# Optimization experiments

Measured on AMD Instinct MI355X. Metric: run time of the kernel, lower is better.

The kernel has to match this reference:

```python
import jax, jax.numpy as jnp
import numpy as np

N = 50000   # nodes
E = 300000  # edges
D = 256     # emb_dim
L = 5       # num_layers
BN_EPS = 1e-5


def setup_inputs() -> dict:
    key = jax.random.key(0)
    ks = jax.random.split(key, 6)
    scale = 0.05
    return {
        "x": jax.random.normal(ks[0], (N, D), jnp.float32),
        "src": jax.random.randint(ks[1], (E,), 0, N, dtype=jnp.int32),
        "dst": jax.random.randint(ks[2], (E,), 0, N, dtype=jnp.int32),
        "W1": jax.random.normal(ks[3], (L, D, D), jnp.float32) * scale,
        "b1": jnp.zeros((L, D), jnp.float32),
        "g1": jnp.ones((L, D), jnp.float32),
        "bt1": jnp.zeros((L, D), jnp.float32),
        "W2": jax.random.normal(ks[4], (L, D, D), jnp.float32) * scale,
        "b2": jnp.zeros((L, D), jnp.float32),
        "eps": jnp.zeros((L,), jnp.float32),
        "bn_g": jnp.ones((L, D), jnp.float32),
        "bn_b": jnp.zeros((L, D), jnp.float32),
    }


def _bn(h, gamma, beta):
    # torch BatchNorm1d training-mode forward: biased batch stats over nodes
    mean = jnp.mean(h, axis=0)
    var = jnp.var(h, axis=0)
    return (h - mean) * jax.lax.rsqrt(var + BN_EPS) * gamma + beta


def reference(x, src, dst, W1, b1, g1, bt1, W2, b2, eps, bn_g, bn_b):
    h = x
    for l in range(L):
        # GINConv: gather relu(x[src]) -> scatter-sum to dst
        msg = jax.nn.relu(h[src])                          # [E, D]
        agg = jax.ops.segment_sum(msg, dst, num_segments=N)  # [N, D]
        z = (1.0 + eps[l]) * h + agg
        # mlp: Linear -> BN -> ReLU -> Linear
        z = z @ W1[l] + b1[l]
        z = jax.nn.relu(_bn(z, g1[l], bt1[l]))
        z = z @ W2[l] + b2[l]
        # per-layer BatchNorm; dropout is identity (eval / drop_ratio=0)
        z = _bn(z, bn_g[l], bn_b[l])
        if l < L - 1:
            z = jax.nn.relu(z)
        h = z
    return h  # JK='last'
```

## Files before the change

### kernel.cpp

```cpp
#include <hip/hip_runtime.h>
#include <hip/hip_bf16.h>

#define N_NODES 50000
#define N_EDGES 300000
#define DIM 256
#define MPAD 50048

typedef __attribute__((ext_vector_type(8))) _Float16 half8;
typedef __attribute__((ext_vector_type(4))) _Float16 half4;
typedef __attribute__((ext_vector_type(4))) float f32x4;

__device__ __forceinline__ void async16(const void* g, void* l) {
    __builtin_amdgcn_global_load_lds(
        (const __attribute__((address_space(1))) unsigned int*)g,
        (__attribute__((address_space(3))) unsigned int*)l, 16, 0, 0);
}

__global__ __launch_bounds__(256) void hist_dst(const int* __restrict__ dst,
                                                int* __restrict__ deg, int E) {
    int e = blockIdx.x * blockDim.x + threadIdx.x;
    if (e < E) atomicAdd(&deg[dst[e]], 1);
}

__global__ __launch_bounds__(1024) void scan_blk(const int* __restrict__ deg,
                                                 int* __restrict__ ptr,
                                                 int* __restrict__ bsum, int n) {
    __shared__ int wsum[16];
    __shared__ int wpre[16];
    int tid = threadIdx.x;
    int i = blockIdx.x * 1024 + tid;
    int v = (i < n) ? deg[i] : 0;
    int lane = tid & 63, w = tid >> 6;
    int s = v;
#pragma unroll
    for (int off = 1; off < 64; off <<= 1) {
        int t = __shfl_up(s, off, 64);
        if (lane >= off) s += t;
    }
    if (lane == 63) wsum[w] = s;
    __syncthreads();
    if (tid < 16) {
        int acc = 0;
        for (int j = 0; j < tid; j++) acc += wsum[j];
        wpre[tid] = acc;
    }
    __syncthreads();
    int incl = s + wpre[w];
    if (i < n) ptr[i] = incl - v;
    if (tid == 1023) bsum[blockIdx.x] = incl;
}

__global__ __launch_bounds__(64) void scan_top(int* __restrict__ bsum,
                                               int* __restrict__ ptr,
                                               int nb, int n, int E) {
    int lane = threadIdx.x;
    int v = (lane < nb) ? bsum[lane] : 0;
    int s = v;
#pragma unroll
    for (int off = 1; off < 64; off <<= 1) {
        int t = __shfl_up(s, off, 64);
        if (lane >= off) s += t;
    }
    if (lane < nb) bsum[lane] = s - v;
    if (lane == 0) ptr[n] = E;
}

__global__ __launch_bounds__(1024) void scan_add(int* __restrict__ ptr,
                                                 const int* __restrict__ bsum,
                                                 int* __restrict__ cursor, int n) {
    int i = blockIdx.x * 1024 + threadIdx.x;
    if (i < n) {
        int val = ptr[i] + bsum[blockIdx.x];
        ptr[i] = val;
        cursor[i] = val;
    }
}

__global__ __launch_bounds__(256) void scatter_src(const int* __restrict__ src,
                                                   const int* __restrict__ dst,
                                                   int* __restrict__ cursor,
                                                   int* __restrict__ srcbuf, int E) {
    int e = blockIdx.x * blockDim.x + threadIdx.x;
    if (e < E) {
        int pos = atomicAdd(&cursor[dst[e]], 1);
        srcbuf[pos] = src[e];
    }
}

__global__ __launch_bounds__(256) void x2h(const float* __restrict__ x,
                                           _Float16* __restrict__ hb) {
    size_t i = (size_t)blockIdx.x * 256 + threadIdx.x;
    float4 v = ((const float4*)x)[i];
    half4 o;
    o.x = (_Float16)v.x; o.y = (_Float16)v.y;
    o.z = (_Float16)v.z; o.w = (_Float16)v.w;
    ((half4*)hb)[i] = o;
}

__global__ __launch_bounds__(256) void wconv(const float* __restrict__ W1,
                                             const float* __restrict__ W2,
                                             _Float16* __restrict__ Wt) {
    int mat = blockIdx.x >> 4;
    int t = blockIdx.x & 15;
    int tr = t >> 2, tc = t & 3;
    const float* W = (mat < 5) ? (W1 + (size_t)mat * 65536)
                               : (W2 + (size_t)(mat - 5) * 65536);
    __shared__ float tile[64][65];
    int tid = threadIdx.x;
    int c = tid & 63, r0 = tid >> 6;
#pragma unroll 4
    for (int i = 0; i < 16; i++) {
        int r = r0 + i * 4;
        tile[r][c] = W[(size_t)(tr * 64 + r) * 256 + tc * 64 + c];
    }
    __syncthreads();
    _Float16* o = Wt + (size_t)mat * 65536;
#pragma unroll 4
    for (int i = 0; i < 16; i++) {
        int r = r0 + i * 4;
        o[(size_t)(tc * 64 + r) * 256 + tr * 64 + c] = (_Float16)tile[c][r];
    }
}

__global__ __launch_bounds__(256) void gather_h(const _Float16* __restrict__ h,
                                                const int* __restrict__ ptr,
                                                const int* __restrict__ srcbuf,
                                                _Float16* __restrict__ z,
                                                const float* __restrict__ eps) {
    int node = blockIdx.x * 4 + (threadIdx.x >> 6);
    if (node >= N_NODES) return;
    int lane = threadIdx.x & 63;
    int beg = ptr[node], end = ptr[node + 1];
    float s = 1.0f + eps[0];
    half4 hv = ((const half4*)(h + (size_t)node * DIM))[lane];
    float a0 = (float)hv.x * s, a1 = (float)hv.y * s;
    float a2 = (float)hv.z * s, a3 = (float)hv.w * s;
    int e = beg;
    for (; e + 4 <= end; e += 4) {
        int s0 = srcbuf[e], s1 = srcbuf[e + 1], s2 = srcbuf[e + 2], s3 = srcbuf[e + 3];
        half4 v0 = ((const half4*)(h + (size_t)s0 * DIM))[lane];
        half4 v1 = ((const half4*)(h + (size_t)s1 * DIM))[lane];
        half4 v2 = ((const half4*)(h + (size_t)s2 * DIM))[lane];
        half4 v3 = ((const half4*)(h + (size_t)s3 * DIM))[lane];
        a0 += fmaxf((float)v0.x, 0.f) + fmaxf((float)v1.x, 0.f)
            + fmaxf((float)v2.x, 0.f) + fmaxf((float)v3.x, 0.f);
        a1 += fmaxf((float)v0.y, 0.f) + fmaxf((float)v1.y, 0.f)
            + fmaxf((float)v2.y, 0.f) + fmaxf((float)v3.y, 0.f);
        a2 += fmaxf((float)v0.z, 0.f) + fmaxf((float)v1.z, 0.f)
            + fmaxf((float)v2.z, 0.f) + fmaxf((float)v3.z, 0.f);
        a3 += fmaxf((float)v0.w, 0.f) + fmaxf((float)v1.w, 0.f)
            + fmaxf((float)v2.w, 0.f) + fmaxf((float)v3.w, 0.f);
    }
    for (; e < end; e++) {
        half4 v = ((const half4*)(h + (size_t)srcbuf[e] * DIM))[lane];
        a0 += fmaxf((float)v.x, 0.f); a1 += fmaxf((float)v.y, 0.f);
        a2 += fmaxf((float)v.z, 0.f); a3 += fmaxf((float)v.w, 0.f);
    }
    half4 o;
    o.x = (_Float16)a0; o.y = (_Float16)a1;
    o.z = (_Float16)a2; o.w = (_Float16)a3;
    ((half4*)(z + (size_t)node * DIM))[lane] = o;
}

__global__ __launch_bounds__(256) void gather_bn(const _Float16* __restrict__ C,
                                                 const int* __restrict__ ptr,
                                                 const int* __restrict__ srcbuf,
                                                 _Float16* __restrict__ z,
                                                 const float* __restrict__ scsh,
                                                 const float* __restrict__ eps,
                                                 int l) {
    int node = blockIdx.x * 4 + (threadIdx.x >> 6);
    if (node >= N_NODES) return;
    int lane = threadIdx.x & 63;
    float4 sc = ((const float4*)scsh)[lane];
    float4 sh = ((const float4*)(scsh + DIM))[lane];
    int beg = ptr[node], end = ptr[node + 1];
    float s = 1.0f + eps[l];
    half4 hv = ((const half4*)(C + (size_t)node * DIM))[lane];
    float a0 = s * fmaxf((float)hv.x * sc.x + sh.x, 0.f);
    float a1 = s * fmaxf((float)hv.y * sc.y + sh.y, 0.f);
    float a2 = s * fmaxf((float)hv.z * sc.z + sh.z, 0.f);
    float a3 = s * fmaxf((float)hv.w * sc.w + sh.w, 0.f);
    int e = beg;
    for (; e + 4 <= end; e += 4) {
        int s0 = srcbuf[e], s1 = srcbuf[e + 1], s2 = srcbuf[e + 2], s3 = srcbuf[e + 3];
        half4 v0 = ((const half4*)(C + (size_t)s0 * DIM))[lane];
        half4 v1 = ((const half4*)(C + (size_t)s1 * DIM))[lane];
        half4 v2 = ((const half4*)(C + (size_t)s2 * DIM))[lane];
        half4 v3 = ((const half4*)(C + (size_t)s3 * DIM))[lane];
        a0 += fmaxf((float)v0.x * sc.x + sh.x, 0.f) + fmaxf((float)v1.x * sc.x + sh.x, 0.f)
            + fmaxf((float)v2.x * sc.x + sh.x, 0.f) + fmaxf((float)v3.x * sc.x + sh.x, 0.f);
        a1 += fmaxf((float)v0.y * sc.y + sh.y, 0.f) + fmaxf((float)v1.y * sc.y + sh.y, 0.f)
            + fmaxf((float)v2.y * sc.y + sh.y, 0.f) + fmaxf((float)v3.y * sc.y + sh.y, 0.f);
        a2 += fmaxf((float)v0.z * sc.z + sh.z, 0.f) + fmaxf((float)v1.z * sc.z + sh.z, 0.f)
            + fmaxf((float)v2.z * sc.z + sh.z, 0.f) + fmaxf((float)v3.z * sc.z + sh.z, 0.f);
        a3 += fmaxf((float)v0.w * sc.w + sh.w, 0.f) + fmaxf((float)v1.w * sc.w + sh.w, 0.f)
            + fmaxf((float)v2.w * sc.w + sh.w, 0.f) + fmaxf((float)v3.w * sc.w + sh.w, 0.f);
    }
    for (; e < end; e++) {
        half4 v = ((const half4*)(C + (size_t)srcbuf[e] * DIM))[lane];
        a0 += fmaxf((float)v.x * sc.x + sh.x, 0.f);
        a1 += fmaxf((float)v.y * sc.y + sh.y, 0.f);
        a2 += fmaxf((float)v.z * sc.z + sh.z, 0.f);
        a3 += fmaxf((float)v.w * sc.w + sh.w, 0.f);
    }
    half4 o;
    o.x = (_Float16)a0; o.y = (_Float16)a1;
    o.z = (_Float16)a2; o.w = (_Float16)a3;
    ((half4*)(z + (size_t)node * DIM))[lane] = o;
}

#define GEMM_EPILOGUE                                                        \
    __syncthreads();                                                         \
    float* colsum = (float*)((char*)smem + 49152);                           \
    float* colsq = colsum + 128;                                             \
    if (tid < 128) { colsum[tid] = 0.0f; colsq[tid] = 0.0f; }                \
    _Float16* Cs = (_Float16*)smem;                                          \
    float bcol[4];                                                           \
    _Pragma("unroll")                                                        \
    for (int j = 0; j < 4; j++) bcol[j] = bias[col0 + wn + j * 16 + lrow];   \
    float csum[4] = {0.f, 0.f, 0.f, 0.f};                                    \
    float csq[4] = {0.f, 0.f, 0.f, 0.f};                                     \
    _Pragma("unroll")                                                        \
    for (int i = 0; i < 4; i++) {                                            \
        int rl = wm + i * 16 + quad * 4;                                     \
        _Pragma("unroll")                                                    \
        for (int j = 0; j < 4; j++) {                                        \
            int cl = wn + j * 16 + lrow;                                     \
            _Pragma("unroll")                                                \
            for (int r = 0; r < 4; r++) {                                    \
                float v = acc[i][j][r] + bcol[j];                            \
                Cs[(rl + r) * 136 + cl] = (_Float16)v;                       \
                if (row0 + rl + r < M) { csum[j] += v; csq[j] += v * v; }    \
            }                                                                \
        }                                                                    \
    }                                                                        \
    __syncthreads();                                                         \
    {                                                                        \
        int rgrp = lane >> 4, ch = lane & 15;                                \
        _Pragma("unroll")                                                    \
        for (int it = 0; it < 8; it++) {                                     \
            int row = wid * 32 + it * 4 + rgrp;                              \
            uint4 vv = *(const uint4*)(Cs + row * 136 + ch * 8);             \
            *(uint4*)(C + (size_t)(row0 + row) * DIM + col0 + ch * 8) = vv;  \
        }                                                                    \
    }                                                                        \
    _Pragma("unroll")                                                        \
    for (int j = 0; j < 4; j++) {                                            \
        atomicAdd(&colsum[wn + j * 16 + lrow], csum[j]);                     \
        atomicAdd(&colsq[wn + j * 16 + lrow], csq[j]);                       \
    }                                                                        \
    __syncthreads();                                                         \
    if (tid < 128) {                                                         \
        float* st = stats + (blockIdx.y & 7) * 512;                          \
        atomicAdd(&st[col0 + tid], colsum[tid]);                             \
        atomicAdd(&st[DIM + col0 + tid], colsq[tid]);                        \
    }

__global__ __launch_bounds__(256) void gemm_f16(const _Float16* __restrict__ A,
                                                const _Float16* __restrict__ Wt,
                                                const float* __restrict__ bias,
                                                _Float16* __restrict__ C,
                                                float* __restrict__ stats,
                                                int M) {
    __shared__ uint4 smem[4096];

    int tid = threadIdx.x;
    int wid = tid >> 6, lane = tid & 63;
    int quad = lane >> 4, lrow = lane & 15;
    int row0 = blockIdx.y * 128, col0 = blockIdx.x * 128;
    int wm = (wid & 1) * 64, wn = (wid >> 1) * 64;

    f32x4 acc[4][4] = {};
    const char* Ab = (const char*)A;
    const char* Bb = (const char*)Wt;

#pragma unroll
    for (int ko = 0; ko < 2; ko++) {
        int kb0 = ko * 256;
#pragma unroll
        for (int j = 0; j < 8; j++) {
            int sbase = wid * 512 + j * 64;
            int s = sbase + lane;
            int m = s >> 4;
            int c = (s & 15) ^ (m & 7);
            size_t go = (size_t)(row0 + m) * 512 + kb0 + c * 16;
            async16(Ab + go, (char*)smem + sbase * 16);
            size_t gob = (size_t)(col0 + m) * 512 + kb0 + c * 16;
            async16(Bb + gob, (char*)smem + 32768 + sbase * 16);
        }
        __syncthreads();
#pragma unroll
        for (int kc = 0; kc < 4; kc++) {
            half8 af[4], bf[4];
#pragma unroll
            for (int t = 0; t < 4; t++) {
                int ma = wm + t * 16 + lrow;
                int ca = kc * 4 + quad;
                af[t] = *(const half8*)((const char*)smem +
                                        (ma * 16 + (ca ^ (ma & 7))) * 16);
                int mb = wn + t * 16 + lrow;
                bf[t] = *(const half8*)((const char*)smem + 32768 +
                                        (mb * 16 + (ca ^ (mb & 7))) * 16);
            }
#pragma unroll
            for (int i = 0; i < 4; i++)
#pragma unroll
                for (int j2 = 0; j2 < 4; j2++)
                    acc[i][j2] = __builtin_amdgcn_mfma_f32_16x16x32_f16(
                        af[i], bf[j2], acc[i][j2], 0, 0, 0);
        }
        if (ko == 0) __syncthreads();
    }

    GEMM_EPILOGUE
}

__global__ __launch_bounds__(256) void gemm_bn(const _Float16* __restrict__ A,
                                               const _Float16* __restrict__ Wt,
                                               const float* __restrict__ bias,
                                               const float* __restrict__ scsh,
                                               _Float16* __restrict__ C,
                                               float* __restrict__ stats,
                                               int M) {
    __shared__ uint4 smem[4096];

    int tid = threadIdx.x;
    int wid = tid >> 6, lane = tid & 63;
    int quad = lane >> 4, lrow = lane & 15;
    int row0 = blockIdx.y * 128, col0 = blockIdx.x * 128;
    int wm = (wid & 1) * 64, wn = (wid >> 1) * 64;

    half8 scv[8], shv[8];
#pragma unroll
    for (int cc = 0; cc < 8; cc++) {
        int kk = cc * 32 + quad * 8;
        float4 s0 = *(const float4*)(scsh + kk);
        float4 s1 = *(const float4*)(scsh + kk + 4);
        float4 h0 = *(const float4*)(scsh + DIM + kk);
        float4 h1 = *(const float4*)(scsh + DIM + kk + 4);
        half8 sv = {(_Float16)s0.x, (_Float16)s0.y, (_Float16)s0.z, (_Float16)s0.w,
                    (_Float16)s1.x, (_Float16)s1.y, (_Float16)s1.z, (_Float16)s1.w};
        half8 hv = {(_Float16)h0.x, (_Float16)h0.y, (_Float16)h0.z, (_Float16)h0.w,
                    (_Float16)h1.x, (_Float16)h1.y, (_Float16)h1.z, (_Float16)h1.w};
        scv[cc] = sv;
        shv[cc] = hv;
    }

    f32x4 acc[4][4] = {};
    const char* Ab = (const char*)A;
    const char* Bb = (const char*)Wt;
    const half8 zerov = {0, 0, 0, 0, 0, 0, 0, 0};

#pragma unroll
    for (int ko = 0; ko < 2; ko++) {
        int kb0 = ko * 256;
#pragma unroll
        for (int j = 0; j < 8; j++) {
            int sbase = wid * 512 + j * 64;
            int s = sbase + lane;
            int m = s >> 4;
            int c = (s & 15) ^ (m & 7);
            size_t go = (size_t)(row0 + m) * 512 + kb0 + c * 16;
            async16(Ab + go, (char*)smem + sbase * 16);
            size_t gob = (size_t)(col0 + m) * 512 + kb0 + c * 16;
            async16(Bb + gob, (char*)smem + 32768 + sbase * 16);
        }
        __syncthreads();
#pragma unroll
        for (int kc = 0; kc < 4; kc++) {
            half8 af[4], bf[4];
            half8 sv = scv[ko * 4 + kc];
            half8 hv = shv[ko * 4 + kc];
#pragma unroll
            for (int t = 0; t < 4; t++) {
                int ma = wm + t * 16 + lrow;
                int ca = kc * 4 + quad;
                half8 a = *(const half8*)((const char*)smem +
                                          (ma * 16 + (ca ^ (ma & 7))) * 16);
                af[t] = __builtin_elementwise_max(a * sv + hv, zerov);
                int mb = wn + t * 16 + lrow;
                bf[t] = *(const half8*)((const char*)smem + 32768 +
                                        (mb * 16 + (ca ^ (mb & 7))) * 16);
            }
#pragma unroll
            for (int i = 0; i < 4; i++)
#pragma unroll
                for (int j2 = 0; j2 < 4; j2++)
                    acc[i][j2] = __builtin_amdgcn_mfma_f32_16x16x32_f16(
                        af[i], bf[j2], acc[i][j2], 0, 0, 0);
        }
        if (ko == 0) __syncthreads();
    }

    GEMM_EPILOGUE
}

__global__ __launch_bounds__(256) void bn_finalize(float* __restrict__ stats,
                                                   const float* __restrict__ g,
                                                   const float* __restrict__ beta,
                                                   float* __restrict__ scsh,
                                                   int n) {
    int d = threadIdx.x;
    float s = 0.0f, sq = 0.0f;
#pragma unroll
    for (int r = 0; r < 8; r++) {
        s += stats[r * 512 + d];
        sq += stats[r * 512 + 256 + d];
        stats[r * 512 + d] = 0.0f;
        stats[r * 512 + 256 + d] = 0.0f;
    }
    float invn = 1.0f / (float)n;
    float mean = s * invn;
    float var = sq * invn - mean * mean;
    float inv = rsqrtf(var + 1e-5f);
    float scale = g[d] * inv;
    scsh[d] = scale;
    scsh[DIM + d] = beta[d] - mean * scale;
}

__global__ __launch_bounds__(256) void bn_apply_f(const _Float16* __restrict__ in,
                                                  float* __restrict__ outf,
                                                  const float* __restrict__ scsh) {
    size_t i = (size_t)blockIdx.x * 256 + threadIdx.x;
    int c4 = (int)(i & 63);
    float4 sc = ((const float4*)scsh)[c4];
    float4 sh = ((const float4*)(scsh + DIM))[c4];
    half4 v = ((const half4*)in)[i];
    float4 o;
    o.x = (float)v.x * sc.x + sh.x;
    o.y = (float)v.y * sc.y + sh.y;
    o.z = (float)v.z * sc.z + sh.z;
    o.w = (float)v.w * sc.w + sh.w;
    ((float4*)outf)[i] = o;
}

extern "C" void kernel_launch(void* const* d_in, const int* in_sizes, int n_in,
                              void* d_out, int out_size, void* d_ws, size_t ws_size,
                              hipStream_t stream) {
    (void)in_sizes; (void)n_in; (void)out_size; (void)ws_size;
    const float* x   = (const float*)d_in[0];
    const int*   src = (const int*)d_in[1];
    const int*   dst = (const int*)d_in[2];
    const float* W1  = (const float*)d_in[3];
    const float* b1  = (const float*)d_in[4];
    const float* g1  = (const float*)d_in[5];
    const float* bt1 = (const float*)d_in[6];
    const float* W2  = (const float*)d_in[7];
    const float* b2  = (const float*)d_in[8];
    const float* eps = (const float*)d_in[9];
    const float* bng = (const float*)d_in[10];
    const float* bnb = (const float*)d_in[11];
    float* out = (float*)d_out;

    const int N = N_NODES, E = N_EDGES, D = DIM;
    size_t NDp = (size_t)MPAD * D;

    _Float16* gin  = (_Float16*)d_ws;
    _Float16* C1   = gin + NDp;
    _Float16* C2   = C1 + NDp;
    _Float16* Wt   = C2 + NDp;
    float* statsA = (float*)(Wt + 10 * 65536);
    float* statsB = statsA + 4096;
    float* scshA = statsB + 4096;
    float* scshB = scshA + 512;
    int* deg     = (int*)(scshB + 512);
    int* ptr     = deg + N;
    int* bsum    = ptr + N + 1;
    int* srcbuf  = bsum + 64;

    const int ELEM4_BLOCKS = N * D / 4 / 256;
    const int NODE_BLOCKS  = (N + 3) / 4;
    const int E_BLOCKS     = (E + 255) / 256;
    const int SCAN_BLOCKS  = (N + 1023) / 1024;
    const dim3 GEMM_GRID(2, MPAD / 128);

    hipMemsetAsync(deg, 0, N * sizeof(int), stream);
    hipMemsetAsync(statsA, 0, 8192 * sizeof(float), stream);
    hist_dst<<<E_BLOCKS, 256, 0, stream>>>(dst, deg, E);
    scan_blk<<<SCAN_BLOCKS, 1024, 0, stream>>>(deg, ptr, bsum, N);
    scan_top<<<1, 64, 0, stream>>>(bsum, ptr, SCAN_BLOCKS, N, E);
    scan_add<<<SCAN_BLOCKS, 1024, 0, stream>>>(ptr, bsum, deg, N);
    scatter_src<<<E_BLOCKS, 256, 0, stream>>>(src, dst, deg, srcbuf, E);
    wconv<<<160, 256, 0, stream>>>(W1, W2, Wt);
    x2h<<<ELEM4_BLOCKS, 256, 0, stream>>>(x, C1);

    for (int l = 0; l < 5; l++) {
        if (l == 0)
            gather_h<<<NODE_BLOCKS, 256, 0, stream>>>(C1, ptr, srcbuf, gin, eps);
        else
            gather_bn<<<NODE_BLOCKS, 256, 0, stream>>>(C2, ptr, srcbuf, gin,
                                                       scshB, eps, l);

        gemm_f16<<<GEMM_GRID, 256, 0, stream>>>(
            gin, Wt + (size_t)l * 65536, b1 + (size_t)l * D, C1, statsA, N);
        bn_finalize<<<1, 256, 0, stream>>>(statsA, g1 + (size_t)l * D,
                                           bt1 + (size_t)l * D, scshA, N);

        gemm_bn<<<GEMM_GRID, 256, 0, stream>>>(
            C1, Wt + (size_t)(5 + l) * 65536, b2 + (size_t)l * D, scshA,
            C2, statsB, N);
        bn_finalize<<<1, 256, 0, stream>>>(statsB, bng + (size_t)l * D,
                                           bnb + (size_t)l * D, scshB, N);

        if (l == 4)
            bn_apply_f<<<ELEM4_BLOCKS, 256, 0, stream>>>(C2, out, scshB);
    }
}
```

Baseline: 674.5 us.

## Shrink GEMM LDS tiles to K=64 chunks, merge setup kernels and memsets

The two GEMM kernels now stream K in four 64-element chunks instead of two 128-element chunks. This roughly halves their shared memory (about 35 KB instead of 64 KB) so more blocks can be resident per CU, at the cost of extra barriers and less work per load phase. Separately, the scan_top kernel is folded into scan_add, which now computes each block's prefix offset by a wave reduction. The weight-convert and x-to-fp16 kernels are merged into one launch, and the two memsets are combined by placing deg right after the stats buffers. Together these changes cut kernel launch count in the setup phase.

```diff
diff --git a/kernel.cpp b/kernel.cpp
--- a/kernel.cpp
+++ b/kernel.cpp
@@ -50,30 +50,26 @@
     if (tid == 1023) bsum[blockIdx.x] = incl;
 }
 
-__global__ __launch_bounds__(64) void scan_top(int* __restrict__ bsum,
-                                               int* __restrict__ ptr,
-                                               int nb, int n, int E) {
-    int lane = threadIdx.x;
-    int v = (lane < nb) ? bsum[lane] : 0;
-    int s = v;
-#pragma unroll
-    for (int off = 1; off < 64; off <<= 1) {
-        int t = __shfl_up(s, off, 64);
-        if (lane >= off) s += t;
-    }
-    if (lane < nb) bsum[lane] = s - v;
-    if (lane == 0) ptr[n] = E;
-}
-
 __global__ __launch_bounds__(1024) void scan_add(int* __restrict__ ptr,
                                                  const int* __restrict__ bsum,
-                                                 int* __restrict__ cursor, int n) {
-    int i = blockIdx.x * 1024 + threadIdx.x;
+                                                 int* __restrict__ cursor,
+                                                 int n, int E) {
+    __shared__ int soff;
+    int tid = threadIdx.x;
+    if (tid < 64) {
+        int v = (tid < (int)blockIdx.x) ? bsum[tid] : 0;
+#pragma unroll
+        for (int off = 32; off > 0; off >>= 1) v += __shfl_down(v, off, 64);
+        if (tid == 0) soff = v;
+    }
+    __syncthreads();
+    int i = blockIdx.x * 1024 + tid;
     if (i < n) {
-        int val = ptr[i] + bsum[blockIdx.x];
+        int val = ptr[i] + soff;
         ptr[i] = val;
         cursor[i] = val;
     }
+    if (i == n) ptr[n] = E;
 }
 
 __global__ __launch_bounds__(256) void scatter_src(const int* __restrict__ src,
@@ -87,38 +83,39 @@
     }
 }
 
-__global__ __launch_bounds__(256) void x2h(const float* __restrict__ x,
-                                           _Float16* __restrict__ hb) {
-    size_t i = (size_t)blockIdx.x * 256 + threadIdx.x;
-    float4 v = ((const float4*)x)[i];
-    half4 o;
-    o.x = (_Float16)v.x; o.y = (_Float16)v.y;
-    o.z = (_Float16)v.z; o.w = (_Float16)v.w;
-    ((half4*)hb)[i] = o;
-}
-
-__global__ __launch_bounds__(256) void wconv(const float* __restrict__ W1,
-                                             const float* __restrict__ W2,
-                                             _Float16* __restrict__ Wt) {
-    int mat = blockIdx.x >> 4;
-    int t = blockIdx.x & 15;
-    int tr = t >> 2, tc = t & 3;
-    const float* W = (mat < 5) ? (W1 + (size_t)mat * 65536)
-                               : (W2 + (size_t)(mat - 5) * 65536);
+__global__ __launch_bounds__(256) void prep(const float* __restrict__ W1,
+                                            const float* __restrict__ W2,
+                                            _Float16* __restrict__ Wt,
+                                            const float* __restrict__ x,
+                                            _Float16* __restrict__ hb) {
     __shared__ float tile[64][65];
     int tid = threadIdx.x;
-    int c = tid & 63, r0 = tid >> 6;
+    if (blockIdx.x < 160) {
+        int mat = blockIdx.x >> 4;
+        int t = blockIdx.x & 15;
+        int tr = t >> 2, tc = t & 3;
+        const float* W = (mat < 5) ? (W1 + (size_t)mat * 65536)
+                                   : (W2 + (size_t)(mat - 5) * 65536);
+        int c = tid & 63, r0 = tid >> 6;
 #pragma unroll 4
-    for (int i = 0; i < 16; i++) {
-        int r = r0 + i * 4;
-        tile[r][c] = W[(size_t)(tr * 64 + r) * 256 + tc * 64 + c];
-    }
-    __syncthreads();
-    _Float16* o = Wt + (size_t)mat * 65536;
+        for (int i = 0; i < 16; i++) {
+            int r = r0 + i * 4;
+            tile[r][c] = W[(size_t)(tr * 64 + r) * 256 + tc * 64 + c];
+        }
+        __syncthreads();
+        _Float16* o = Wt + (size_t)mat * 65536;
 #pragma unroll 4
-    for (int i = 0; i < 16; i++) {
-        int r = r0 + i * 4;
-        o[(size_t)(tc * 64 + r) * 256 + tr * 64 + c] = (_Float16)tile[c][r];
+        for (int i = 0; i < 16; i++) {
+            int r = r0 + i * 4;
+            o[(size_t)(tc * 64 + r) * 256 + tr * 64 + c] = (_Float16)tile[c][r];
+        }
+    } else {
+        size_t i = (size_t)(blockIdx.x - 160) * 256 + tid;
+        float4 v = ((const float4*)x)[i];
+        half4 o;
+        o.x = (_Float16)v.x; o.y = (_Float16)v.y;
+        o.z = (_Float16)v.z; o.w = (_Float16)v.w;
+        ((half4*)hb)[i] = o;
     }
 }
 
@@ -212,7 +209,7 @@
 
 #define GEMM_EPILOGUE                                                        \
     __syncthreads();                                                         \
-    float* colsum = (float*)((char*)smem + 49152);                           \
+    float* colsum = (float*)((char*)smem + 34816);                           \
     float* colsq = colsum + 128;                                             \
     if (tid < 128) { colsum[tid] = 0.0f; colsq[tid] = 0.0f; }                \
     _Float16* Cs = (_Float16*)smem;                                          \
@@ -263,7 +260,7 @@
                                                 _Float16* __restrict__ C,
                                                 float* __restrict__ stats,
                                                 int M) {
-    __shared__ uint4 smem[4096];
+    __shared__ uint4 smem[2240];
 
     int tid = threadIdx.x;
     int wid = tid >> 6, lane = tid & 63;
@@ -276,32 +273,32 @@
     const char* Bb = (const char*)Wt;
 
 #pragma unroll
-    for (int ko = 0; ko < 2; ko++) {
-        int kb0 = ko * 256;
-#pragma unroll
-        for (int j = 0; j < 8; j++) {
-            int sbase = wid * 512 + j * 64;
+    for (int ko = 0; ko < 4; ko++) {
+        int kb0 = ko * 128;
+#pragma unroll
+        for (int j = 0; j < 4; j++) {
+            int sbase = wid * 256 + j * 64;
             int s = sbase + lane;
-            int m = s >> 4;
-            int c = (s & 15) ^ (m & 7);
+            int m = s >> 3;
+            int c = (s & 7) ^ (m & 7);
             size_t go = (size_t)(row0 + m) * 512 + kb0 + c * 16;
             async16(Ab + go, (char*)smem + sbase * 16);
             size_t gob = (size_t)(col0 + m) * 512 + kb0 + c * 16;
-            async16(Bb + gob, (char*)smem + 32768 + sbase * 16);
+            async16(Bb + gob, (char*)smem + 16384 + sbase * 16);
         }
         __syncthreads();
 #pragma unroll
-        for (int kc = 0; kc < 4; kc++) {
+        for (int kc = 0; kc < 2; kc++) {
             half8 af[4], bf[4];
 #pragma unroll
             for (int t = 0; t < 4; t++) {
                 int ma = wm + t * 16 + lrow;
                 int ca = kc * 4 + quad;
                 af[t] = *(const half8*)((const char*)smem +
-                                        (ma * 16 + (ca ^ (ma & 7))) * 16);
+                                        (ma * 8 + (ca ^ (ma & 7))) * 16);
                 int mb = wn + t * 16 + lrow;
-                bf[t] = *(const half8*)((const char*)smem + 32768 +
-                                        (mb * 16 + (ca ^ (mb & 7))) * 16);
+                bf[t] = *(const half8*)((const char*)smem + 16384 +
+                                        (mb * 8 + (ca ^ (mb & 7))) * 16);
             }
 #pragma unroll
             for (int i = 0; i < 4; i++)
@@ -310,7 +307,7 @@
                     acc[i][j2] = __builtin_amdgcn_mfma_f32_16x16x32_f16(
                         af[i], bf[j2], acc[i][j2], 0, 0, 0);
         }
-        if (ko == 0) __syncthreads();
+        if (ko < 3) __syncthreads();
     }
 
     GEMM_EPILOGUE
@@ -323,7 +320,7 @@
                                                _Float16* __restrict__ C,
                                                float* __restrict__ stats,
                                                int M) {
-    __shared__ uint4 smem[4096];
+    __shared__ uint4 smem[2240];
 
     int tid = threadIdx.x;
     int wid = tid >> 6, lane = tid & 63;
@@ -353,35 +350,35 @@
     const half8 zerov = {0, 0, 0, 0, 0, 0, 0, 0};
 
 #pragma unroll
-    for (int ko = 0; ko < 2; ko++) {
-        int kb0 = ko * 256;
-#pragma unroll
-        for (int j = 0; j < 8; j++) {
-            int sbase = wid * 512 + j * 64;
+    for (int ko = 0; ko < 4; ko++) {
+        int kb0 = ko * 128;
+#pragma unroll
+        for (int j = 0; j < 4; j++) {
+            int sbase = wid * 256 + j * 64;
             int s = sbase + lane;
-            int m = s >> 4;
-            int c = (s & 15) ^ (m & 7);
+            int m = s >> 3;
+            int c = (s & 7) ^ (m & 7);
             size_t go = (size_t)(row0 + m) * 512 + kb0 + c * 16;
             async16(Ab + go, (char*)smem + sbase * 16);
             size_t gob = (size_t)(col0 + m) * 512 + kb0 + c * 16;
-            async16(Bb + gob, (char*)smem + 32768 + sbase * 16);
+            async16(Bb + gob, (char*)smem + 16384 + sbase * 16);
         }
         __syncthreads();
 #pragma unroll
-        for (int kc = 0; kc < 4; kc++) {
+        for (int kc = 0; kc < 2; kc++) {
             half8 af[4], bf[4];
-            half8 sv = scv[ko * 4 + kc];
-            half8 hv = shv[ko * 4 + kc];
+            half8 sv = scv[ko * 2 + kc];
+            half8 hv = shv[ko * 2 + kc];
 #pragma unroll
             for (int t = 0; t < 4; t++) {
                 int ma = wm + t * 16 + lrow;
                 int ca = kc * 4 + quad;
                 half8 a = *(const half8*)((const char*)smem +
-                                          (ma * 16 + (ca ^ (ma & 7))) * 16);
+                                          (ma * 8 + (ca ^ (ma & 7))) * 16);
                 af[t] = __builtin_elementwise_max(a * sv + hv, zerov);
                 int mb = wn + t * 16 + lrow;
-                bf[t] = *(const half8*)((const char*)smem + 32768 +
-                                        (mb * 16 + (ca ^ (mb & 7))) * 16);
+                bf[t] = *(const half8*)((const char*)smem + 16384 +
+                                        (mb * 8 + (ca ^ (mb & 7))) * 16);
             }
 #pragma unroll
             for (int i = 0; i < 4; i++)
@@ -390,7 +387,7 @@
                     acc[i][j2] = __builtin_amdgcn_mfma_f32_16x16x32_f16(
                         af[i], bf[j2], acc[i][j2], 0, 0, 0);
         }
-        if (ko == 0) __syncthreads();
+        if (ko < 3) __syncthreads();
     }
 
     GEMM_EPILOGUE
@@ -460,14 +457,14 @@
     _Float16* C1   = gin + NDp;
     _Float16* C2   = C1 + NDp;
     _Float16* Wt   = C2 + NDp;
-    float* statsA = (float*)(Wt + 10 * 65536);
-    float* statsB = statsA + 4096;
-    float* scshA = statsB + 4096;
-    float* scshB = scshA + 512;
-    int* deg     = (int*)(scshB + 512);
-    int* ptr     = deg + N;
-    int* bsum    = ptr + N + 1;
-    int* srcbuf  = bsum + 64;
+    float* statsA  = (float*)(Wt + 10 * 65536);
+    float* statsB  = statsA + 4096;
+    int* deg       = (int*)(statsB + 4096);
+    int* ptr       = deg + N;
+    int* bsum      = ptr + N + 1;
+    int* srcbuf    = bsum + 64;
+    float* scshA   = (float*)(srcbuf + E);
+    float* scshB   = scshA + 512;
 
     const int ELEM4_BLOCKS = N * D / 4 / 256;
     const int NODE_BLOCKS  = (N + 3) / 4;
@@ -475,15 +472,12 @@
     const int SCAN_BLOCKS  = (N + 1023) / 1024;
     const dim3 GEMM_GRID(2, MPAD / 128);
 
-    hipMemsetAsync(deg, 0, N * sizeof(int), stream);
-    hipMemsetAsync(statsA, 0, 8192 * sizeof(float), stream);
+    hipMemsetAsync(statsA, 0, (size_t)(8192 + N) * sizeof(float), stream);
     hist_dst<<<E_BLOCKS, 256, 0, stream>>>(dst, deg, E);
     scan_blk<<<SCAN_BLOCKS, 1024, 0, stream>>>(deg, ptr, bsum, N);
-    scan_top<<<1, 64, 0, stream>>>(bsum, ptr, SCAN_BLOCKS, N, E);
-    scan_add<<<SCAN_BLOCKS, 1024, 0, stream>>>(ptr, bsum, deg, N);
+    scan_add<<<SCAN_BLOCKS, 1024, 0, stream>>>(ptr, bsum, deg, N, E);
     scatter_src<<<E_BLOCKS, 256, 0, stream>>>(src, dst, deg, srcbuf, E);
-    wconv<<<160, 256, 0, stream>>>(W1, W2, Wt);
-    x2h<<<ELEM4_BLOCKS, 256, 0, stream>>>(x, C1);
+    prep<<<160 + ELEM4_BLOCKS, 256, 0, stream>>>(W1, W2, Wt, x, C1);
 
     for (int l = 0; l < 5; l++) {
         if (l == 0)
```

Result: faster. 628.3 us (-6.9%).
